# Performance work log

Hardware: AMD Instinct MI355X
Metric: run time of the kernel (lower is better)

Reference implementation:

```python
import jax, jax.numpy as jnp
import numpy as np

N, K, D, P, B = 16384, 64, 128, 8, 32
LN_EPS = 1e-5


def _silu(x):
    return x * jax.nn.sigmoid(x)


def setup_inputs() -> dict:
    key = jax.random.key(0)
    ks = jax.random.split(key, 12)
    s = 1.0 / np.sqrt(D)
    return {
        "x_scalar": jax.random.normal(ks[0], (N, D), jnp.float32),
        "k_dot_r": jax.random.normal(ks[1], (N, K), jnp.float32) * 3.0,
        "sinc_damping": jax.random.uniform(ks[2], (N, K), jnp.float32),
        "batch": jnp.sort(jax.random.randint(ks[3], (N,), 0, B)),
        "down_projection": jax.random.normal(ks[4], (K, P), jnp.float32),
        "W_pre1": jax.random.normal(ks[5], (D, D), jnp.float32) * s,
        "W_pre2": jax.random.normal(ks[6], (D, D), jnp.float32) * s,
        "ln_gamma": jnp.ones((D,), jnp.float32),
        "ln_beta": jnp.zeros((D,), jnp.float32),
        "W_up": jax.random.normal(ks[7], (D, P), jnp.float32) * (1.0 / np.sqrt(P)) * 0.01,
        "W_upd1": jax.random.normal(ks[8], (D, D), jnp.float32) * s,
        "W_upd2": jax.random.normal(ks[9], (D, D), jnp.float32) * s,
    }


def reference(x_scalar, k_dot_r, sinc_damping, batch, down_projection,
              W_pre1, W_pre2, ln_gamma, ln_beta, W_up, W_upd1, W_upd2):
    # pre_mlp residual: x + act(act(x W1^T) W2^T)
    h = _silu(_silu(x_scalar @ W_pre1.T) @ W_pre2.T)
    x_res = x_scalar + h
    # LayerNorm over feature dim
    mu = jnp.mean(x_res, axis=-1, keepdims=True)
    var = jnp.mean(jnp.square(x_res - mu), axis=-1, keepdims=True)
    x_res = (x_res - mu) * jax.lax.rsqrt(var + LN_EPS) * ln_gamma + ln_beta
    # trig structure factors
    real = jnp.cos(k_dot_r) * sinc_damping  # [N, K]
    imag = jnp.sin(k_dot_r) * sinc_damping  # [N, K]
    # scatter-sum per graph: sf[b,k,d] = sum_{n in b} trig[n,k] * x_res[n,d]
    sf_real = jax.ops.segment_sum(real[:, :, None] * x_res[:, None, :], batch, num_segments=B)
    sf_imag = jax.ops.segment_sum(imag[:, :, None] * x_res[:, None, :], batch, num_segments=B)
    # k-space filter: [K, D]
    kfilter = down_projection @ W_up.T
    # gather back per node and reduce over K
    fr = (kfilter[None, :, :] * sf_real)[batch]  # [N, K, D]
    fi = (kfilter[None, :, :] * sf_imag)[batch]  # [N, K, D]
    ewald_message = jnp.einsum('nkd,nk->nd', fr, real) + jnp.einsum('nkd,nk->nd', fi, imag)
    x = x_scalar + ewald_message
    return x + _silu(_silu(x @ W_upd1.T) @ W_upd2.T)
```

## Files before the change

kernel.cpp:

```cpp
#include <hip/hip_runtime.h>
#include <stdint.h>

#define NN 16384
#define KK 64
#define DD 128
#define PP 8
#define NB 32
#define CH 64
#define CHD 32

typedef unsigned short ushort_t;
typedef __attribute__((ext_vector_type(8))) short short8;
typedef __attribute__((ext_vector_type(4))) float f32x4;

__device__ __forceinline__ ushort_t f2bf(float x) {
    unsigned u = __float_as_uint(x);
    u += 0x7fffu + ((u >> 16) & 1u);
    return (ushort_t)(u >> 16);
}
__device__ __forceinline__ float silu_f(float v) { return v / (1.0f + __expf(-v)); }

__device__ __forceinline__ short8 ldWf(const float* __restrict__ W, int row, int col) {
    float4 a = *(const float4*)&W[(size_t)row * DD + col];
    float4 b = *(const float4*)&W[(size_t)row * DD + col + 4];
    short8 v;
    v[0] = (short)f2bf(a.x); v[1] = (short)f2bf(a.y);
    v[2] = (short)f2bf(a.z); v[3] = (short)f2bf(a.w);
    v[4] = (short)f2bf(b.x); v[5] = (short)f2bf(b.y);
    v[6] = (short)f2bf(b.z); v[7] = (short)f2bf(b.w);
    return v;
}

__global__ __launch_bounds__(256, 4) void kB_pre(
        const float* __restrict__ x, const float* __restrict__ W1,
        const float* __restrict__ W2, const float* __restrict__ W3,
        const float* __restrict__ W4, const float* __restrict__ gamma,
        const float* __restrict__ beta, const float* __restrict__ kdr,
        const float* __restrict__ damp, const int* __restrict__ batch,
        ushort_t* __restrict__ Wb, int* __restrict__ starts_g,
        ushort_t* __restrict__ trig_rm, ushort_t* __restrict__ trigTb,
        ushort_t* __restrict__ xresTb) {
    __shared__ __align__(16) ushort_t xsb[16][136];
    __shared__ __align__(16) ushort_t t1b[16][136];
    __shared__ float2 lnp[16][4];
    const int bid = blockIdx.x;

    if (bid < 8) {
        int w = bid;
        const float* s = ((w >> 2) == 0 ? W3 : W4) + (w & 3) * 4096;
        ushort_t* d = Wb + (size_t)(w >> 2) * 16384 + (w & 3) * 4096;
        for (int i = threadIdx.x; i < 4096; i += 256) d[i] = f2bf(s[i]);
        return;
    }
    if (bid == 8) {
        const int t = threadIdx.x;
        if (t <= NB) {
            int lo;
            if (t == NB) lo = NN;
            else {
                lo = 0; int hi = NN;
                while (lo < hi) { int mid = (lo + hi) >> 1; if (batch[mid] < t) lo = mid + 1; else hi = mid; }
            }
            starts_g[t] = lo;
        }
        return;
    }

    const int t = threadIdx.x, lane = t & 63, wv = t >> 6;
    const int ci = bid - 9;
    const int n0 = ci * 16;

    float2 kvp[2], dvp[2];
#pragma unroll
    for (int q = 0; q < 2; ++q) {
        int i = t + q * 256;
        int r = i >> 5, kk = (i & 31) * 2;
        kvp[q] = *(const float2*)&kdr[(size_t)(n0 + r) * KK + kk];
        dvp[q] = *(const float2*)&damp[(size_t)(n0 + r) * KK + kk];
    }
    {
        const float4* src = (const float4*)(x + (size_t)n0 * DD);
        float4 v0 = src[t * 2], v1 = src[t * 2 + 1];
        int r = t >> 4, c = (t & 15) << 3;
        short8 pk;
        pk[0] = (short)f2bf(v0.x); pk[1] = (short)f2bf(v0.y);
        pk[2] = (short)f2bf(v0.z); pk[3] = (short)f2bf(v0.w);
        pk[4] = (short)f2bf(v1.x); pk[5] = (short)f2bf(v1.y);
        pk[6] = (short)f2bf(v1.z); pk[7] = (short)f2bf(v1.w);
        *(short8*)&xsb[r][c] = pk;
    }
    __syncthreads();

    const int chf = wv * 32;
    const int fr = (lane >> 4) * 8, cr = lane & 15, rr4 = (lane >> 4) * 4;
    f32x4 acc[2];
    const f32x4 z4 = {0.f, 0.f, 0.f, 0.f};

#pragma unroll
    for (int nt = 0; nt < 2; ++nt) acc[nt] = z4;
#pragma unroll
    for (int ks = 0; ks < 4; ++ks) {
        short8 af = *(const short8*)&xsb[cr][ks * 32 + fr];
#pragma unroll
        for (int nt = 0; nt < 2; ++nt) {
            short8 bf = ldWf(W1, chf + nt * 16 + cr, ks * 32 + fr);
            acc[nt] = __builtin_amdgcn_mfma_f32_16x16x32_bf16(af, bf, acc[nt], 0, 0, 0);
        }
    }
#pragma unroll
    for (int nt = 0; nt < 2; ++nt)
#pragma unroll
        for (int r = 0; r < 4; ++r)
            t1b[rr4 + r][chf + nt * 16 + cr] = f2bf(silu_f(acc[nt][r]));
    __syncthreads();

#pragma unroll
    for (int nt = 0; nt < 2; ++nt) acc[nt] = z4;
#pragma unroll
    for (int ks = 0; ks < 4; ++ks) {
        short8 af = *(const short8*)&t1b[cr][ks * 32 + fr];
#pragma unroll
        for (int nt = 0; nt < 2; ++nt) {
            short8 bf = ldWf(W2, chf + nt * 16 + cr, ks * 32 + fr);
            acc[nt] = __builtin_amdgcn_mfma_f32_16x16x32_bf16(af, bf, acc[nt], 0, 0, 0);
        }
    }
#pragma unroll
    for (int q = 0; q < 2; ++q) {
        int i = t + q * 256;
        int r = i >> 5, kk = (i & 31) * 2;
        float s0, c0, s1, c1;
        __sincosf(kvp[q].x, &s0, &c0);
        __sincosf(kvp[q].y, &s1, &c1);
        ushort_t rc0 = f2bf(c0 * dvp[q].x), rc1 = f2bf(c1 * dvp[q].y);
        ushort_t is0 = f2bf(s0 * dvp[q].x), is1 = f2bf(s1 * dvp[q].y);
        xsb[r][kk] = rc0; xsb[r][kk + 1] = rc1;
        xsb[r][64 + kk] = is0; xsb[r][64 + kk + 1] = is1;
        ushort2 a; a.x = rc0; a.y = rc1;
        ushort2 b; b.x = is0; b.y = is1;
        *(ushort2*)&trig_rm[(size_t)(n0 + r) * 128 + kk] = a;
        *(ushort2*)&trig_rm[(size_t)(n0 + r) * 128 + 64 + kk] = b;
    }
    float g[2], be[2];
#pragma unroll
    for (int nt = 0; nt < 2; ++nt) {
        g[nt] = gamma[chf + nt * 16 + cr];
        be[nt] = beta[chf + nt * 16 + cr];
    }
#pragma unroll
    for (int r = 0; r < 4; ++r) {
        int row = n0 + rr4 + r;
        float s = 0.f, sq = 0.f;
#pragma unroll
        for (int nt = 0; nt < 2; ++nt) {
            float v = x[(size_t)row * DD + chf + nt * 16 + cr] + silu_f(acc[nt][r]);
            acc[nt][r] = v;
            s += v; sq += v * v;
        }
#pragma unroll
        for (int off = 1; off < 16; off <<= 1) {
            s += __shfl_xor(s, off);
            sq += __shfl_xor(sq, off);
        }
        if (cr == 0) {
            float2 p; p.x = s; p.y = sq;
            lnp[rr4 + r][wv] = p;
        }
    }
    __syncthreads();

#pragma unroll
    for (int r = 0; r < 4; ++r) {
        int row = rr4 + r;
        float2 a0 = lnp[row][0], a1 = lnp[row][1], a2 = lnp[row][2], a3 = lnp[row][3];
        float s = a0.x + a1.x + a2.x + a3.x, sq = a0.y + a1.y + a2.y + a3.y;
        float mu = s * (1.0f / 128.0f);
        float var = sq * (1.0f / 128.0f) - mu * mu;
        float rs = rsqrtf(var + 1e-5f);
#pragma unroll
        for (int nt = 0; nt < 2; ++nt)
            t1b[row][chf + nt * 16 + cr] = f2bf((acc[nt][r] - mu) * rs * g[nt] + be[nt]);
    }
    __syncthreads();

    {
        int m = t >> 1, hh = (t & 1) * 8;
        size_t base = (size_t)(ci >> 2) * 8192 + (size_t)m * 64 + (ci & 3) * 16 + hh;
        short8 v;
#pragma unroll
        for (int j = 0; j < 8; ++j) v[j] = (short)xsb[hh + j][m];
        *(short8*)&trigTb[base] = v;
#pragma unroll
        for (int j = 0; j < 8; ++j) v[j] = (short)t1b[hh + j][m];
        *(short8*)&xresTb[base] = v;
    }
}

__global__ __launch_bounds__(256, 4) void kS_scatter(
        const int* __restrict__ starts_g,
        const ushort_t* __restrict__ xresTb, const ushort_t* __restrict__ trigTb,
        const float* __restrict__ dp, const float* __restrict__ wup,
        ushort_t* __restrict__ SFTb) {
    __shared__ __align__(16) ushort_t xt[16][72];
    __shared__ __align__(16) ushort_t tt[64][72];
    __shared__ int seg2[2];
    const int b = blockIdx.x & 31, g2 = blockIdx.x >> 5;
    const int d0 = (g2 & 7) * 16, mh = (g2 >> 3) * 64;
    const int t = threadIdx.x, lane = t & 63, wv = t >> 6;

    if (t < 2) seg2[t] = starts_g[b + t];
    __syncthreads();
    const int segs = seg2[0], sege = seg2[1];

    const int fr = (lane >> 4) * 8, cr = lane & 15, rr4 = (lane >> 4) * 4;
    const f32x4 z4 = {0.f, 0.f, 0.f, 0.f};
    f32x4 acc = z4;

    for (int r0 = segs & ~(CH - 1); r0 < sege; r0 += CH) {
        int lo = segs - r0; if (lo < 0) lo = 0;
        int hi = sege - r0; if (hi > CH) hi = CH;
        const size_t cb = (size_t)(r0 >> 6) * 8192;
        for (int i = t; i < 160; i += 256) {
            int row = i >> 1, h = (i & 1) * 32;
            const ushort_t* src = (row < 16 ? xresTb + cb + (size_t)(d0 + row) * 64
                                            : trigTb + cb + (size_t)(mh + row - 16) * 64) + h;
            ushort_t* dst = (row < 16 ? &xt[row][h] : &tt[row - 16][h]);
            if (lo == 0 && hi == CH) {
#pragma unroll
                for (int q = 0; q < 4; ++q) *(short8*)(dst + q * 8) = *(const short8*)(src + q * 8);
            } else {
                for (int j = 0; j < 32; ++j) { int c = h + j; dst[j] = (c >= lo && c < hi) ? src[j] : (ushort_t)0; }
            }
        }
        __syncthreads();
#pragma unroll
        for (int ks = 0; ks < 2; ++ks) {
            short8 af = *(const short8*)&xt[cr][ks * 32 + fr];
            short8 bf = *(const short8*)&tt[wv * 16 + cr][ks * 32 + fr];
            acc = __builtin_amdgcn_mfma_f32_16x16x32_bf16(af, bf, acc, 0, 0, 0);
        }
        __syncthreads();
    }

    const int m = mh + wv * 16 + cr;
    const int k = m & 63;
    float4 p0 = *(const float4*)&dp[k * PP];
    float4 p1 = *(const float4*)&dp[k * PP + 4];
#pragma unroll
    for (int r = 0; r < 4; ++r) {
        int d = d0 + rr4 + r;
        float4 w0 = *(const float4*)&wup[d * PP];
        float4 w1 = *(const float4*)&wup[d * PP + 4];
        float kf = p0.x * w0.x + p0.y * w0.y + p0.z * w0.z + p0.w * w0.w
                 + p1.x * w1.x + p1.y * w1.y + p1.z * w1.z + p1.w * w1.w;
        SFTb[((size_t)b * 128 + d) * 128 + m] = f2bf(acc[r] * kf);
    }
}

__global__ __launch_bounds__(256, 3) void kD_post(
        const float* __restrict__ x, const int* __restrict__ starts_g,
        const ushort_t* __restrict__ trig_rm, const ushort_t* __restrict__ SFTb,
        const ushort_t* __restrict__ Wb, float* __restrict__ out) {
    __shared__ __align__(16) ushort_t sft[128 * 136];
    __shared__ __align__(16) ushort_t xs[32][136];
    __shared__ int starts[NB + 1];
    __shared__ int offs[NB + 1];
    const int t = threadIdx.x, lane = t & 63, wv = t >> 6;
    const int fr = (lane >> 4) * 8, cr = lane & 15, rr4 = (lane >> 4) * 4;
    const f32x4 z4 = {0.f, 0.f, 0.f, 0.f};

    if (t < 33) starts[t] = starts_g[t];
    __syncthreads();
    if (t == 0) {
        int off = 0;
        for (int b = 0; b < NB; ++b) {
            offs[b] = off;
            off += (starts[b + 1] - starts[b] + CHD - 1) / CHD;
        }
        offs[NB] = off;
    }
    __syncthreads();
    const int nwl = offs[NB];
    const int c = (blockIdx.x & 7) * 72 + (blockIdx.x >> 3);
    if (c >= nwl) return;
    int b = 0;
    while (offs[b + 1] <= c) ++b;
    const int r0c = starts[b] + (c - offs[b]) * CHD;
    const int len = min(CHD, starts[b + 1] - r0c);

    const int ar0 = (wv & 1) * 16;
    const int chf = (wv >> 1) * 64;
    const ushort_t* W3b = Wb;
    const ushort_t* W4b = Wb + 16384;

    int nrow = r0c + ar0 + cr; if (nrow >= NN) nrow = NN - 1;
    short8 afp[4];
#pragma unroll
    for (int ks = 0; ks < 4; ++ks)
        afp[ks] = *(const short8*)&trig_rm[(size_t)nrow * 128 + ks * 32 + fr];
    float xr[4][4];
#pragma unroll
    for (int nt = 0; nt < 4; ++nt)
#pragma unroll
        for (int r = 0; r < 4; ++r) {
            int row = r0c + ar0 + rr4 + r; if (row >= NN) row = NN - 1;
            xr[nt][r] = x[(size_t)row * DD + chf + nt * 16 + cr];
        }

    {
        const ushort_t* srcS = SFTb + (size_t)b * 16384;
        for (int i = t; i < 2048; i += 256) {
            int r = i >> 4, cc = (i & 15) * 8;
            *(short8*)&sft[r * 136 + cc] = *(const short8*)(srcS + r * 128 + cc);
        }
    }
    __syncthreads();

    f32x4 g4[4];
#pragma unroll
    for (int nt = 0; nt < 4; ++nt) g4[nt] = z4;
#pragma unroll
    for (int ks = 0; ks < 4; ++ks) {
#pragma unroll
        for (int nt = 0; nt < 4; ++nt) {
            short8 bf = *(const short8*)&sft[(chf + nt * 16 + cr) * 136 + ks * 32 + fr];
            g4[nt] = __builtin_amdgcn_mfma_f32_16x16x32_bf16(afp[ks], bf, g4[nt], 0, 0, 0);
        }
    }

    float xk[4][4];
#pragma unroll
    for (int nt = 0; nt < 4; ++nt)
#pragma unroll
        for (int r = 0; r < 4; ++r) {
            int rr = ar0 + rr4 + r;
            float xv = xr[nt][r] + g4[nt][r];
            xk[nt][r] = xv;
            xs[rr][chf + nt * 16 + cr] = f2bf(xv);
        }
    __syncthreads();

#pragma unroll
    for (int nt = 0; nt < 4; ++nt) g4[nt] = z4;
#pragma unroll
    for (int ks = 0; ks < 4; ++ks) {
        short8 af = *(const short8*)&xs[ar0 + cr][ks * 32 + fr];
#pragma unroll
        for (int nt = 0; nt < 4; ++nt) {
            short8 bf = *(const short8*)&W3b[(size_t)(chf + nt * 16 + cr) * DD + ks * 32 + fr];
            g4[nt] = __builtin_amdgcn_mfma_f32_16x16x32_bf16(af, bf, g4[nt], 0, 0, 0);
        }
    }
#pragma unroll
    for (int nt = 0; nt < 4; ++nt)
#pragma unroll
        for (int r = 0; r < 4; ++r)
            sft[(ar0 + rr4 + r) * 136 + chf + nt * 16 + cr] = f2bf(silu_f(g4[nt][r]));
    __syncthreads();

#pragma unroll
    for (int nt = 0; nt < 4; ++nt) g4[nt] = z4;
#pragma unroll
    for (int ks = 0; ks < 4; ++ks) {
        short8 af = *(const short8*)&sft[(ar0 + cr) * 136 + ks * 32 + fr];
#pragma unroll
        for (int nt = 0; nt < 4; ++nt) {
            short8 bf = *(const short8*)&W4b[(size_t)(chf + nt * 16 + cr) * DD + ks * 32 + fr];
            g4[nt] = __builtin_amdgcn_mfma_f32_16x16x32_bf16(af, bf, g4[nt], 0, 0, 0);
        }
    }
#pragma unroll
    for (int nt = 0; nt < 4; ++nt)
#pragma unroll
        for (int r = 0; r < 4; ++r) {
            int rr = ar0 + rr4 + r;
            if (rr < len)
                out[(size_t)(r0c + rr) * DD + chf + nt * 16 + cr] = xk[nt][r] + silu_f(g4[nt][r]);
        }
}

extern "C" void kernel_launch(void* const* d_in, const int* in_sizes, int n_in,
                              void* d_out, int out_size, void* d_ws, size_t ws_size,
                              hipStream_t stream) {
    const float* x      = (const float*)d_in[0];
    const float* kdr    = (const float*)d_in[1];
    const float* damp   = (const float*)d_in[2];
    const int*   batch  = (const int*)d_in[3];
    const float* dp     = (const float*)d_in[4];
    const float* W_pre1 = (const float*)d_in[5];
    const float* W_pre2 = (const float*)d_in[6];
    const float* gamma  = (const float*)d_in[7];
    const float* beta   = (const float*)d_in[8];
    const float* W_up   = (const float*)d_in[9];
    const float* W_upd1 = (const float*)d_in[10];
    const float* W_upd2 = (const float*)d_in[11];
    float* out = (float*)d_out;

    char* w = (char*)d_ws;
    ushort_t* Wb       = (ushort_t*)w;
    int*      starts_g = (int*)(w + 65536);
    size_t o = 131072;
    ushort_t* trig_rm = (ushort_t*)(w + o);  o += (size_t)NN * 128 * 2;
    ushort_t* trigTb  = (ushort_t*)(w + o);  o += (size_t)NN * 128 * 2;
    ushort_t* xresTb  = (ushort_t*)(w + o);  o += (size_t)NN * 128 * 2;
    ushort_t* SFTb    = (ushort_t*)(w + o);  o += (size_t)NB * 128 * 128 * 2;

    hipLaunchKernelGGL(kB_pre, dim3(9 + NN / 16), dim3(256), 0, stream,
                       x, W_pre1, W_pre2, W_upd1, W_upd2, gamma, beta,
                       kdr, damp, batch, Wb, starts_g, trig_rm, trigTb, xresTb);
    hipLaunchKernelGGL(kS_scatter, dim3(NB * 16), dim3(256), 0, stream,
                       starts_g, xresTb, trigTb, dp, W_up, SFTb);
    hipLaunchKernelGGL(kD_post, dim3(576), dim3(256), 0, stream,
                       x, starts_g, trig_rm, SFTb, Wb, out);
}
```

Measured before the change: 63.17 us.

## Prefetch MLP weight fragments into registers and double-buffer scatter LDS tiles

In the pre-MLP kernel, the W1/W2 bf16 fragments and the residual x values are loaded into registers ahead of the MFMA loops and barriers, so global-load latency overlaps with other work. In the scatter kernel, the LDS staging tiles are double-buffered so the next chunk is loaded while MFMAs run on the current one, which removes one barrier per iteration. This raises register and LDS pressure, which may lower occupancy.

```diff
diff --git a/kernel.cpp b/kernel.cpp
--- a/kernel.cpp
+++ b/kernel.cpp
@@ -69,6 +69,8 @@
     const int t = threadIdx.x, lane = t & 63, wv = t >> 6;
     const int ci = bid - 9;
     const int n0 = ci * 16;
+    const int chf = wv * 32;
+    const int fr = (lane >> 4) * 8, cr = lane & 15, rr4 = (lane >> 4) * 4;
 
     float2 kvp[2], dvp[2];
 #pragma unroll
@@ -78,6 +80,12 @@
         kvp[q] = *(const float2*)&kdr[(size_t)(n0 + r) * KK + kk];
         dvp[q] = *(const float2*)&damp[(size_t)(n0 + r) * KK + kk];
     }
+    short8 w1f[2][4];
+#pragma unroll
+    for (int ks = 0; ks < 4; ++ks)
+#pragma unroll
+        for (int nt = 0; nt < 2; ++nt)
+            w1f[nt][ks] = ldWf(W1, chf + nt * 16 + cr, ks * 32 + fr);
     {
         const float4* src = (const float4*)(x + (size_t)n0 * DD);
         float4 v0 = src[t * 2], v1 = src[t * 2 + 1];
@@ -91,8 +99,6 @@
     }
     __syncthreads();
 
-    const int chf = wv * 32;
-    const int fr = (lane >> 4) * 8, cr = lane & 15, rr4 = (lane >> 4) * 4;
     f32x4 acc[2];
     const f32x4 z4 = {0.f, 0.f, 0.f, 0.f};
 
@@ -102,16 +108,27 @@
     for (int ks = 0; ks < 4; ++ks) {
         short8 af = *(const short8*)&xsb[cr][ks * 32 + fr];
 #pragma unroll
-        for (int nt = 0; nt < 2; ++nt) {
-            short8 bf = ldWf(W1, chf + nt * 16 + cr, ks * 32 + fr);
-            acc[nt] = __builtin_amdgcn_mfma_f32_16x16x32_bf16(af, bf, acc[nt], 0, 0, 0);
-        }
+        for (int nt = 0; nt < 2; ++nt)
+            acc[nt] = __builtin_amdgcn_mfma_f32_16x16x32_bf16(af, w1f[nt][ks], acc[nt], 0, 0, 0);
     }
 #pragma unroll
     for (int nt = 0; nt < 2; ++nt)
 #pragma unroll
         for (int r = 0; r < 4; ++r)
             t1b[rr4 + r][chf + nt * 16 + cr] = f2bf(silu_f(acc[nt][r]));
+
+    short8 w2f[2][4];
+#pragma unroll
+    for (int ks = 0; ks < 4; ++ks)
+#pragma unroll
+        for (int nt = 0; nt < 2; ++nt)
+            w2f[nt][ks] = ldWf(W2, chf + nt * 16 + cr, ks * 32 + fr);
+    float xr[2][4];
+#pragma unroll
+    for (int nt = 0; nt < 2; ++nt)
+#pragma unroll
+        for (int r = 0; r < 4; ++r)
+            xr[nt][r] = x[(size_t)(n0 + rr4 + r) * DD + chf + nt * 16 + cr];
     __syncthreads();
 
 #pragma unroll
@@ -120,10 +137,8 @@
     for (int ks = 0; ks < 4; ++ks) {
         short8 af = *(const short8*)&t1b[cr][ks * 32 + fr];
 #pragma unroll
-        for (int nt = 0; nt < 2; ++nt) {
-            short8 bf = ldWf(W2, chf + nt * 16 + cr, ks * 32 + fr);
-            acc[nt] = __builtin_amdgcn_mfma_f32_16x16x32_bf16(af, bf, acc[nt], 0, 0, 0);
-        }
+        for (int nt = 0; nt < 2; ++nt)
+            acc[nt] = __builtin_amdgcn_mfma_f32_16x16x32_bf16(af, w2f[nt][ks], acc[nt], 0, 0, 0);
     }
 #pragma unroll
     for (int q = 0; q < 2; ++q) {
@@ -149,11 +164,10 @@
     }
 #pragma unroll
     for (int r = 0; r < 4; ++r) {
-        int row = n0 + rr4 + r;
         float s = 0.f, sq = 0.f;
 #pragma unroll
         for (int nt = 0; nt < 2; ++nt) {
-            float v = x[(size_t)row * DD + chf + nt * 16 + cr] + silu_f(acc[nt][r]);
+            float v = xr[nt][r] + silu_f(acc[nt][r]);
             acc[nt][r] = v;
             s += v; sq += v * v;
         }
@@ -201,8 +215,8 @@
         const ushort_t* __restrict__ xresTb, const ushort_t* __restrict__ trigTb,
         const float* __restrict__ dp, const float* __restrict__ wup,
         ushort_t* __restrict__ SFTb) {
-    __shared__ __align__(16) ushort_t xt[16][72];
-    __shared__ __align__(16) ushort_t tt[64][72];
+    __shared__ __align__(16) ushort_t xt[2][16][72];
+    __shared__ __align__(16) ushort_t tt[2][64][72];
     __shared__ int seg2[2];
     const int b = blockIdx.x & 31, g2 = blockIdx.x >> 5;
     const int d0 = (g2 & 7) * 16, mh = (g2 >> 3) * 64;
@@ -211,12 +225,15 @@
     if (t < 2) seg2[t] = starts_g[b + t];
     __syncthreads();
     const int segs = seg2[0], sege = seg2[1];
+    const int base = segs & ~(CH - 1);
+    const int nIter = (sege - base + CH - 1) / CH;
 
     const int fr = (lane >> 4) * 8, cr = lane & 15, rr4 = (lane >> 4) * 4;
     const f32x4 z4 = {0.f, 0.f, 0.f, 0.f};
     f32x4 acc = z4;
 
-    for (int r0 = segs & ~(CH - 1); r0 < sege; r0 += CH) {
+    auto STAGE = [&](int it, int bf) {
+        int r0 = base + it * CH;
         int lo = segs - r0; if (lo < 0) lo = 0;
         int hi = sege - r0; if (hi > CH) hi = CH;
         const size_t cb = (size_t)(r0 >> 6) * 8192;
@@ -224,7 +241,7 @@
             int row = i >> 1, h = (i & 1) * 32;
             const ushort_t* src = (row < 16 ? xresTb + cb + (size_t)(d0 + row) * 64
                                             : trigTb + cb + (size_t)(mh + row - 16) * 64) + h;
-            ushort_t* dst = (row < 16 ? &xt[row][h] : &tt[row - 16][h]);
+            ushort_t* dst = (row < 16 ? &xt[bf][row][h] : &tt[bf][row - 16][h]);
             if (lo == 0 && hi == CH) {
 #pragma unroll
                 for (int q = 0; q < 4; ++q) *(short8*)(dst + q * 8) = *(const short8*)(src + q * 8);
@@ -232,14 +249,22 @@
                 for (int j = 0; j < 32; ++j) { int c = h + j; dst[j] = (c >= lo && c < hi) ? src[j] : (ushort_t)0; }
             }
         }
+    };
+
+    if (nIter > 0) {
+        STAGE(0, 0);
         __syncthreads();
-#pragma unroll
-        for (int ks = 0; ks < 2; ++ks) {
-            short8 af = *(const short8*)&xt[cr][ks * 32 + fr];
-            short8 bf = *(const short8*)&tt[wv * 16 + cr][ks * 32 + fr];
-            acc = __builtin_amdgcn_mfma_f32_16x16x32_bf16(af, bf, acc, 0, 0, 0);
-        }
-        __syncthreads();
+        for (int it = 0; it < nIter; ++it) {
+            int cur = it & 1;
+            if (it + 1 < nIter) STAGE(it + 1, cur ^ 1);
+#pragma unroll
+            for (int ks = 0; ks < 2; ++ks) {
+                short8 af = *(const short8*)&xt[cur][cr][ks * 32 + fr];
+                short8 bf = *(const short8*)&tt[cur][wv * 16 + cr][ks * 32 + fr];
+                acc = __builtin_amdgcn_mfma_f32_16x16x32_bf16(af, bf, acc, 0, 0, 0);
+            }
+            __syncthreads();
+        }
     }
 
     const int m = mh + wv * 16 + cr;
```

Result: no change. 63.47 us (+0.5%).
